# Kernel tuning notes

Measured on AMD Instinct MI355X. Metric: run time of the kernel, lower is better.

The kernel has to match this reference:

```python
import jax, jax.numpy as jnp
import numpy as np
from jax import lax

C = 128; G = 8; K = 3; P = K * K; GC = C // G
N, H, W = 4, 96, 96
EPS = 1e-5

def conv_bn_silu(x, w, gamma, beta, rmean, rvar, stride, pad):
    # Conv2d(bias=False) + BatchNorm2d(eval) + SiLU, NCHW
    y = lax.conv_general_dilated(x, w, (stride, stride), [(pad, pad), (pad, pad)],
                                 dimension_numbers=('NCHW', 'OIHW', 'NCHW'))
    s = gamma / jnp.sqrt(rvar + EPS)
    y = y * s[None, :, None, None] + (beta - rmean * s)[None, :, None, None]
    return y * jax.nn.sigmoid(y)

def dcnv3(x, dw_w, dw_b, ln_g, ln_b, off_w, off_b, m_w, m_b, ip_w, ip_b, op_w, op_b):
    # InternImage DCNv3, channels-last input (N,H,W,C), k=3 s=1 pad=1 dil=1 group=G, offset_scale=1
    n, h, w, c = x.shape
    xp = x @ ip_w.T + ip_b  # input_proj
    # offset/mask branch: depthwise 3x3 conv + LayerNorm + GELU on the ORIGINAL input
    dw = lax.conv_general_dilated(x, dw_w, (1, 1), [(1, 1), (1, 1)],
                                  dimension_numbers=('NHWC', 'HWIO', 'NHWC'),
                                  feature_group_count=c) + dw_b
    dw = (dw - dw.mean(-1, keepdims=True)) / jnp.sqrt(dw.var(-1, keepdims=True) + EPS) * ln_g + ln_b
    dw = jax.nn.gelu(dw)
    off = (dw @ off_w.T + off_b).reshape(n, h, w, G, P, 2)  # (..., (dx, dy))
    m = jax.nn.softmax((dw @ m_w.T + m_b).reshape(n, h, w, G, P), -1)
    pad = 1
    hp, wp = h + 2 * pad, w + 2 * pad
    xpad = jnp.pad(xp, ((0, 0), (pad, pad), (pad, pad), (0, 0))).reshape(n, hp, wp, G, GC)
    ky, kx = jnp.meshgrid(jnp.arange(-1, 2, dtype=x.dtype), jnp.arange(-1, 2, dtype=x.dtype), indexing='ij')
    # absolute sampling coords in padded image (grid_sample align_corners=False equivalent)
    py = (jnp.arange(h, dtype=x.dtype) + pad)[None, :, None, None, None] + ky.reshape(-1) + off[..., 1]
    px = (jnp.arange(w, dtype=x.dtype) + pad)[None, None, :, None, None] + kx.reshape(-1) + off[..., 0]
    yf = jnp.floor(py); xf = jnp.floor(px)
    wy = py - yf; wx = px - xf
    y0 = yf.astype(jnp.int32); x0 = xf.astype(jnp.int32)
    n_idx = jnp.arange(n)[:, None, None, None, None]
    g_idx = jnp.arange(G)[None, None, None, :, None]

    def gat(yi, xi):
        valid = ((yi >= 0) & (yi < hp) & (xi >= 0) & (xi < wp)).astype(x.dtype)
        v = xpad[n_idx, jnp.clip(yi, 0, hp - 1), jnp.clip(xi, 0, wp - 1), g_idx]  # (n,h,w,G,P,GC)
        return v * valid[..., None]

    v = (gat(y0, x0) * ((1 - wy) * (1 - wx))[..., None]
         + gat(y0, x0 + 1) * ((1 - wy) * wx)[..., None]
         + gat(y0 + 1, x0) * (wy * (1 - wx))[..., None]
         + gat(y0 + 1, x0 + 1) * (wy * wx)[..., None])
    out = jnp.einsum('nhwgpc,nhwgp->nhwgc', v, m).reshape(n, h, w, c)
    return out @ op_w.T + op_b  # output_proj

def _forward(x0, x1, x2, conv_w, conv_g, conv_b, conv_rm, conv_rv,
             conv1_w, conv1_g, conv1_b, conv1_rm, conv1_rv,
             conv2_w, conv2_g, conv2_b, conv2_rm, conv2_rv,
             dw_w, dw_b, ln_g, ln_b, off_w, off_b, m_w, m_b, ip_w, ip_b, op_w, op_b):
    n, _, h, w = x0.shape
    # x1: 256 ch > 128 -> self.conv (1x1); smaller spatial -> bilinear upsample to HW
    y1 = conv_bn_silu(x1, conv_w, conv_g, conv_b, conv_rm, conv_rv, 1, 0)
    feat_up1 = jax.image.resize(y1, (n, C, h, w), method='bilinear')
    # x2: 64 ch < 128 -> self.conv1 (1x1); larger spatial -> self.conv2 (3x3 s2) to HW
    y2 = conv_bn_silu(x2, conv1_w, conv1_g, conv1_b, conv1_rm, conv1_rv, 1, 0)
    feat_up2 = conv_bn_silu(y2, conv2_w, conv2_g, conv2_b, conv2_rm, conv2_rv, 2, 1)
    d1 = dcnv3(feat_up1.transpose(0, 2, 3, 1), dw_w, dw_b, ln_g, ln_b, off_w, off_b, m_w, m_b, ip_w, ip_b, op_w, op_b)
    d2 = dcnv3(feat_up2.transpose(0, 2, 3, 1), dw_w, dw_b, ln_g, ln_b, off_w, off_b, m_w, m_b, ip_w, ip_b, op_w, op_b)
    a1 = jax.nn.relu(d1).transpose(0, 3, 1, 2)
    a2 = jax.nn.relu(d2).transpose(0, 3, 1, 2)
    return jnp.concatenate([a1, x0, a2], axis=1)  # (N, 3C, H, W)

def setup_inputs():
    ks = jax.random.split(jax.random.key(0), 24)
    f = jnp.float32
    return {
        'x0': jax.random.normal(ks[0], (N, C, H, W), f),
        'x1': jax.random.normal(ks[1], (N, 2 * C, H // 2, W // 2), f),
        'x2': jax.random.normal(ks[2], (N, C // 2, 2 * H, 2 * W), f),
        'conv_w': jax.random.normal(ks[3], (C, 2 * C, 1, 1), f) * 0.05,
        'conv_g': jnp.ones((C,), f), 'conv_b': jnp.zeros((C,), f),
        'conv_rm': jax.random.normal(ks[4], (C,), f) * 0.1,
        'conv_rv': jax.random.uniform(ks[5], (C,), f) + 0.5,
        'conv1_w': jax.random.normal(ks[6], (C, C // 2, 1, 1), f) * 0.08,
        'conv1_g': jnp.ones((C,), f), 'conv1_b': jnp.zeros((C,), f),
        'conv1_rm': jax.random.normal(ks[7], (C,), f) * 0.1,
        'conv1_rv': jax.random.uniform(ks[8], (C,), f) + 0.5,
        'conv2_w': jax.random.normal(ks[9], (C, C, 3, 3), f) * 0.03,
        'conv2_g': jnp.ones((C,), f), 'conv2_b': jnp.zeros((C,), f),
        'conv2_rm': jax.random.normal(ks[10], (C,), f) * 0.1,
        'conv2_rv': jax.random.uniform(ks[11], (C,), f) + 0.5,
        'dw_w': jax.random.normal(ks[12], (3, 3, 1, C), f) * 0.1,
        'dw_b': jnp.zeros((C,), f),
        'ln_g': jnp.ones((C,), f), 'ln_b': jnp.zeros((C,), f),
        'off_w': jax.random.normal(ks[13], (G * P * 2, C), f) * 0.01,
        'off_b': jnp.zeros((G * P * 2,), f),
        'm_w': jax.random.normal(ks[14], (G * P, C), f) * 0.05,
        'm_b': jnp.zeros((G * P,), f),
        'ip_w': jax.random.normal(ks[15], (C, C), f) * 0.05,
        'ip_b': jnp.zeros((C,), f),
        'op_w': jax.random.normal(ks[16], (C, C), f) * 0.05,
        'op_b': jnp.zeros((C,), f),
    }

def reference(x0, x1, x2, conv_w, conv_g, conv_b, conv_rm, conv_rv,
              conv1_w, conv1_g, conv1_b, conv1_rm, conv1_rv,
              conv2_w, conv2_g, conv2_b, conv2_rm, conv2_rv,
              dw_w, dw_b, ln_g, ln_b, off_w, off_b, m_w, m_b, ip_w, ip_b, op_w, op_b):
    return _forward(x0, x1, x2, conv_w, conv_g, conv_b, conv_rm, conv_rv,
                    conv1_w, conv1_g, conv1_b, conv1_rm, conv1_rv,
                    conv2_w, conv2_g, conv2_b, conv2_rm, conv2_rv,
                    dw_w, dw_b, ln_g, ln_b, off_w, off_b, m_w, m_b, ip_w, ip_b, op_w, op_b)
```

## Files before the change

kernel.cpp:

```cpp
#include <hip/hip_runtime.h>
#include <cstdint>
#include <cstddef>

#define EPSV 1e-5f
#define NPIX 9216
#define LDA 136
#define LDK 72

typedef __bf16 bf16;
typedef __attribute__((ext_vector_type(8))) __bf16 bf16x8;
typedef __attribute__((ext_vector_type(4))) __bf16 bf16x4;
typedef __attribute__((ext_vector_type(4))) float  f32x4;

__device__ __forceinline__ float silu_f(float v) { return v / (1.f + __expf(-v)); }

__global__ __launch_bounds__(256) void prep_kernel(
    const float* __restrict__ conv_w, const float* __restrict__ conv_g,
    const float* __restrict__ conv_b, const float* __restrict__ conv_rm, const float* __restrict__ conv_rv,
    const float* __restrict__ conv1_w, const float* __restrict__ conv1_g,
    const float* __restrict__ conv1_b, const float* __restrict__ conv1_rm, const float* __restrict__ conv1_rv,
    const float* __restrict__ conv2_w, const float* __restrict__ conv2_g,
    const float* __restrict__ conv2_bb, const float* __restrict__ conv2_rm, const float* __restrict__ conv2_rv,
    const float* __restrict__ ip_w, const float* __restrict__ op_w,
    const float* __restrict__ off_w, const float* __restrict__ m_w,
    const float* __restrict__ off_b, const float* __restrict__ m_b,
    float* __restrict__ WTSf, bf16* __restrict__ WTSb)
{
  int idx = blockIdx.x * 256 + threadIdx.x;
  if (idx < 608) {
    if (idx < 128) {
      int co = idx;
      float s = conv_g[co] * rsqrtf(conv_rv[co] + EPSV);
      WTSf[idx] = conv_b[co] - conv_rm[co] * s;
    } else if (idx < 256) {
      int co = idx - 128;
      float s = conv1_g[co] * rsqrtf(conv1_rv[co] + EPSV);
      WTSf[idx] = conv1_b[co] - conv1_rm[co] * s;
    } else if (idx < 384) {
      int co = idx - 256;
      float s = conv2_g[co] * rsqrtf(conv2_rv[co] + EPSV);
      WTSf[idx] = conv2_bb[co] - conv2_rm[co] * s;
    } else {
      int col = idx - 384;
      WTSf[idx] = (col < 144) ? off_b[col] : (col < 216 ? m_b[col - 144] : 0.f);
    }
  } else {
    int j = idx - 608;
    if (j < 32768) {
      int co = j >> 8, ci = j & 255;
      float s = conv_g[co] * rsqrtf(conv_rv[co] + EPSV);
      WTSb[j] = (bf16)(conv_w[co * 256 + ci] * s);
    } else if (j < 40960) {
      int r = j - 32768; int co = r >> 6, ci = r & 63;
      float s = conv1_g[co] * rsqrtf(conv1_rv[co] + EPSV);
      WTSb[j] = (bf16)(conv1_w[co * 64 + ci] * s);
    } else if (j < 188416) {
      int r = j - 40960; int kp = r >> 14; int rr = r & 16383;
      int co = rr >> 7, ci = rr & 127;
      float s = conv2_g[co] * rsqrtf(conv2_rv[co] + EPSV);
      WTSb[j] = (bf16)(conv2_w[(co * 128 + ci) * 9 + kp] * s);
    } else if (j < 204800) {
      int r = j - 188416; int co = r >> 7, ci = r & 127;
      WTSb[j] = (bf16)ip_w[co * 128 + ci];
    } else if (j < 233472) {
      int r = j - 204800; int co = r >> 7, ci = r & 127;
      float v = (co < 144) ? off_w[co * 128 + ci] : (co < 216 ? m_w[(co - 144) * 128 + ci] : 0.f);
      WTSb[j] = (bf16)v;
    } else if (j < 249856) {
      int r = j - 233472; int co = r >> 7, ci = r & 127;
      WTSb[j] = (bf16)op_w[co * 128 + ci];
    }
  }
}

__global__ __launch_bounds__(256) void c1x1_mfma_kernel(
    const float* __restrict__ x, const bf16* __restrict__ W,
    const float* __restrict__ bias, int K, int HW, bf16* __restrict__ outb)
{
  __shared__ bf16 As[64 * LDK];
  __shared__ bf16 Bs[128 * LDK];
  int m0 = blockIdx.x << 6;
  int t = threadIdx.x;
  int n = m0 / HW; int hw0 = m0 - n * HW;
  const float* xn = x + (size_t)n * K * HW;
  int wv = t >> 6, lane = t & 63;
  int lrow = lane & 15, q = lane >> 4;
  int n0 = wv * 32;
  f32x4 acc[4][2];
#pragma unroll
  for (int i = 0; i < 4; ++i)
#pragma unroll
    for (int j = 0; j < 2; ++j)
#pragma unroll
      for (int e = 0; e < 4; ++e) acc[i][j][e] = 0.f;

  for (int k0 = 0; k0 < K; k0 += 64) {
    if (k0) __syncthreads();
    for (int i = t; i < 1024; i += 256) {
      int px = i & 63; int ci4 = (i >> 6) << 2;
      bf16x4 p;
#pragma unroll
      for (int j = 0; j < 4; ++j)
        p[j] = (bf16)xn[(size_t)(k0 + ci4 + j) * HW + hw0 + px];
      *(bf16x4*)&As[px * LDK + ci4] = p;
    }
    for (int i = t; i < 1024; i += 256) {
      int co = i >> 3; int k8 = (i & 7) << 3;
      *(bf16x8*)&Bs[co * LDK + k8] = *(const bf16x8*)&W[(size_t)co * K + k0 + k8];
    }
    __syncthreads();
#pragma unroll
    for (int ks = 0; ks < 2; ++ks) {
      int ko = ks * 32 + q * 8;
      bf16x8 bfr0 = *(const bf16x8*)&Bs[(n0 + lrow) * LDK + ko];
      bf16x8 bfr1 = *(const bf16x8*)&Bs[(n0 + 16 + lrow) * LDK + ko];
#pragma unroll
      for (int mi = 0; mi < 4; ++mi) {
        bf16x8 afr = *(const bf16x8*)&As[(mi * 16 + lrow) * LDK + ko];
        acc[mi][0] = __builtin_amdgcn_mfma_f32_16x16x32_bf16(afr, bfr0, acc[mi][0], 0, 0, 0);
        acc[mi][1] = __builtin_amdgcn_mfma_f32_16x16x32_bf16(afr, bfr1, acc[mi][1], 0, 0, 0);
      }
    }
  }
#pragma unroll
  for (int mi = 0; mi < 4; ++mi) {
#pragma unroll
    for (int nj = 0; nj < 2; ++nj) {
      int co = n0 + nj * 16 + lrow;
      float bb = bias[co];
#pragma unroll
      for (int r = 0; r < 4; ++r) {
        int m = m0 + mi * 16 + q * 4 + r;
        outb[(size_t)m * 128 + co] = (bf16)silu_f(acc[mi][nj][r] + bb);
      }
    }
  }
}

__global__ __launch_bounds__(256) void upsample_kernel(
    const bf16* __restrict__ y1b, bf16* __restrict__ feat1b)
{
  int idx = blockIdx.x * 256 + threadIdx.x;
  int c4 = (idx & 31) << 2;
  int pw = idx >> 5;
  int ow = pw % 96; int t1 = pw / 96;
  int oh = t1 % 96; int n = t1 / 96;
  float sh = oh * 0.5f - 0.25f, sw = ow * 0.5f - 0.25f;
  float hf = floorf(sh), wf = floorf(sw);
  float fy = sh - hf, fx = sw - wf;
  int h0 = (int)hf, w0 = (int)wf;
  int h0c = max(h0, 0), h1c = min(h0 + 1, 47);
  int w0c = max(w0, 0), w1c = min(w0 + 1, 47);
  const bf16* yn = y1b + (size_t)n * 2304 * 128 + c4;
  bf16x4 v00 = *(const bf16x4*)&yn[(h0c * 48 + w0c) * 128];
  bf16x4 v01 = *(const bf16x4*)&yn[(h0c * 48 + w1c) * 128];
  bf16x4 v10 = *(const bf16x4*)&yn[(h1c * 48 + w0c) * 128];
  bf16x4 v11 = *(const bf16x4*)&yn[(h1c * 48 + w1c) * 128];
  bf16x4 o;
#pragma unroll
  for (int e = 0; e < 4; ++e) {
    float v = (1.f - fy) * ((1.f - fx) * (float)v00[e] + fx * (float)v01[e])
            + fy * ((1.f - fx) * (float)v10[e] + fx * (float)v11[e]);
    o[e] = (bf16)v;
  }
  *(bf16x4*)&feat1b[((size_t)n * NPIX + oh * 96 + ow) * 128 + c4] = o;
}

__global__ __launch_bounds__(256) void conv2_mfma_kernel(
    const bf16* __restrict__ y2b, const bf16* __restrict__ W2b,
    const float* __restrict__ b2, bf16* __restrict__ feat2b)
{
  __shared__ bf16 As[64 * LDA];
  __shared__ bf16 Bs[128 * LDA];
  int m0 = blockIdx.x << 6;
  int t = threadIdx.x;
  int wv = t >> 6, lane = t & 63;
  int lrow = lane & 15, q = lane >> 4;
  int n0 = wv * 32;
  f32x4 acc[4][2];
#pragma unroll
  for (int i = 0; i < 4; ++i)
#pragma unroll
    for (int j = 0; j < 2; ++j)
#pragma unroll
      for (int e = 0; e < 4; ++e) acc[i][j][e] = 0.f;
  bf16x8 zv;
#pragma unroll
  for (int e = 0; e < 8; ++e) zv[e] = (bf16)0.f;

  for (int kp = 0; kp < 9; ++kp) {
    int kh = kp / 3, kw = kp - kh * 3;
    __syncthreads();
    for (int i = t; i < 1024; i += 256) {
      int row = i >> 4; int c8 = (i & 15) << 3;
      int m = m0 + row;
      int nimg = m / NPIX; int hw = m - nimg * NPIX;
      int oh = hw / 96, ow = hw - oh * 96;
      int ih = 2 * oh - 1 + kh, iw = 2 * ow - 1 + kw;
      bf16x8 v = zv;
      if ((unsigned)ih < 192u && (unsigned)iw < 192u)
        v = *(const bf16x8*)&y2b[(((size_t)nimg * 192 + ih) * 192 + iw) * 128 + c8];
      *(bf16x8*)&As[row * LDA + c8] = v;
    }
    const bf16* Wk = W2b + kp * 16384;
    for (int i = t; i < 2048; i += 256) {
      int nn = i >> 4; int k8 = (i & 15) << 3;
      *(bf16x8*)&Bs[nn * LDA + k8] = *(const bf16x8*)&Wk[nn * 128 + k8];
    }
    __syncthreads();
#pragma unroll
    for (int ks = 0; ks < 4; ++ks) {
      bf16x8 bfr0 = *(const bf16x8*)&Bs[(n0 + lrow) * LDA + ks * 32 + q * 8];
      bf16x8 bfr1 = *(const bf16x8*)&Bs[(n0 + 16 + lrow) * LDA + ks * 32 + q * 8];
#pragma unroll
      for (int mi = 0; mi < 4; ++mi) {
        bf16x8 afr = *(const bf16x8*)&As[(mi * 16 + lrow) * LDA + ks * 32 + q * 8];
        acc[mi][0] = __builtin_amdgcn_mfma_f32_16x16x32_bf16(afr, bfr0, acc[mi][0], 0, 0, 0);
        acc[mi][1] = __builtin_amdgcn_mfma_f32_16x16x32_bf16(afr, bfr1, acc[mi][1], 0, 0, 0);
      }
    }
  }
#pragma unroll
  for (int mi = 0; mi < 4; ++mi) {
#pragma unroll
    for (int nj = 0; nj < 2; ++nj) {
      int co = n0 + nj * 16 + lrow;
      float bb = b2[co];
#pragma unroll
      for (int r = 0; r < 4; ++r) {
        int m = m0 + mi * 16 + q * 4 + r;
        feat2b[(size_t)m * 128 + co] = (bf16)silu_f(acc[mi][nj][r] + bb);
      }
    }
  }
}

__global__ __launch_bounds__(256) void mm_bf16_kernel(
    const bf16* __restrict__ A, const bf16* __restrict__ W,
    const float* __restrict__ bias, int Nc, int ostride, int act,
    int store_mode, void* __restrict__ outp)
{
  __shared__ bf16 As[64 * LDA];
  __shared__ bf16 Bs[128 * LDA];
  int m0 = blockIdx.x << 6;
  int nb = blockIdx.y << 7;
  int cols_here = Nc - nb; if (cols_here > 128) cols_here = 128;
  int t = threadIdx.x;
  for (int i = t; i < 1024; i += 256) {
    int row = i >> 4; int c8 = (i & 15) << 3;
    *(bf16x8*)&As[row * LDA + c8] = *(const bf16x8*)&A[(size_t)(m0 + row) * 128 + c8];
  }
  bf16x8 zv;
#pragma unroll
  for (int e = 0; e < 8; ++e) zv[e] = (bf16)0.f;
  for (int i = t; i < 2048; i += 256) {
    int n = i >> 4; int k8 = (i & 15) << 3;
    bf16x8 v = (n < cols_here) ? *(const bf16x8*)&W[(size_t)(nb + n) * 128 + k8] : zv;
    *(bf16x8*)&Bs[n * LDA + k8] = v;
  }
  __syncthreads();

  int wv = t >> 6, lane = t & 63;
  int lrow = lane & 15, q = lane >> 4;
  int n0 = wv * 32;
  f32x4 acc[4][2];
#pragma unroll
  for (int i = 0; i < 4; ++i)
#pragma unroll
    for (int j = 0; j < 2; ++j)
#pragma unroll
      for (int e = 0; e < 4; ++e) acc[i][j][e] = 0.f;

#pragma unroll
  for (int ks = 0; ks < 4; ++ks) {
    bf16x8 bfr0 = *(const bf16x8*)&Bs[(n0 + lrow) * LDA + ks * 32 + q * 8];
    bf16x8 bfr1 = *(const bf16x8*)&Bs[(n0 + 16 + lrow) * LDA + ks * 32 + q * 8];
#pragma unroll
    for (int mi = 0; mi < 4; ++mi) {
      bf16x8 afr = *(const bf16x8*)&As[(mi * 16 + lrow) * LDA + ks * 32 + q * 8];
      acc[mi][0] = __builtin_amdgcn_mfma_f32_16x16x32_bf16(afr, bfr0, acc[mi][0], 0, 0, 0);
      acc[mi][1] = __builtin_amdgcn_mfma_f32_16x16x32_bf16(afr, bfr1, acc[mi][1], 0, 0, 0);
    }
  }

  float* outf = (float*)outp;
  bf16*  outb = (bf16*)outp;
#pragma unroll
  for (int mi = 0; mi < 4; ++mi) {
#pragma unroll
    for (int nj = 0; nj < 2; ++nj) {
      int col = nb + n0 + nj * 16 + lrow;
      if (col >= Nc) continue;
      float bb = bias[col];
#pragma unroll
      for (int r = 0; r < 4; ++r) {
        int m = m0 + mi * 16 + q * 4 + r;
        float v = acc[mi][nj][r] + bb;
        if (act == 1) v = fmaxf(v, 0.f);
        if (store_mode == 0) {
          outf[(size_t)m * ostride + col] = v;
        } else if (store_mode == 2) {
          outb[(size_t)m * 128 + col] = (bf16)v;
        } else {
          int nn = m / NPIX; int hw = m - nn * NPIX;
          int img = nn & 3; int choff = (nn >= 4) ? 256 : 0;
          outf[((size_t)(img * 384 + choff + col)) * NPIX + hw] = v;
        }
      }
    }
  }
}

__global__ __launch_bounds__(256) void dwln_kernel(
    const bf16* __restrict__ featb, const float* __restrict__ dw_w,
    const float* __restrict__ dw_b, const float* __restrict__ ln_g,
    const float* __restrict__ ln_b, bf16* __restrict__ dwgb)
{
  int t = threadIdx.x;
  int pxl = t >> 4;
  int c8 = (t & 15) << 3;
  int pixel = blockIdx.x * 16 + pxl;
  int n = pixel / NPIX; int hw = pixel - n * NPIX;
  int h = hw / 96; int w = hw - h * 96;
  const bf16* fn = featb + (size_t)n * NPIX * 128 + c8;
  float acc[8];
#pragma unroll
  for (int e = 0; e < 8; ++e) acc[e] = dw_b[c8 + e];
#pragma unroll
  for (int kh = 0; kh < 3; ++kh) {
    int hh = h + kh - 1;
    if ((unsigned)hh >= 96u) continue;
#pragma unroll
    for (int kw = 0; kw < 3; ++kw) {
      int ww = w + kw - 1;
      if ((unsigned)ww >= 96u) continue;
      bf16x8 v = *(const bf16x8*)&fn[(hh * 96 + ww) * 128];
      const float* wt = &dw_w[(kh * 3 + kw) * 128 + c8];
#pragma unroll
      for (int e = 0; e < 8; ++e) acc[e] += (float)v[e] * wt[e];
    }
  }
  float s = 0.f, qs = 0.f;
#pragma unroll
  for (int e = 0; e < 8; ++e) { s += acc[e]; qs += acc[e] * acc[e]; }
#pragma unroll
  for (int off = 8; off > 0; off >>= 1) {
    s  += __shfl_xor(s, off);
    qs += __shfl_xor(qs, off);
  }
  float mean = s * (1.f / 128.f);
  float var = qs * (1.f / 128.f) - mean * mean;
  float rstd = rsqrtf(var + EPSV);
  bf16x8 o;
#pragma unroll
  for (int e = 0; e < 8; ++e) {
    float xn = (acc[e] - mean) * rstd * ln_g[c8 + e] + ln_b[c8 + e];
    float z = 0.7978845608028654f * (xn + 0.044715f * xn * xn * xn);
    float th;
    if (z > 15.f) th = 1.f;
    else if (z < -15.f) th = -1.f;
    else { float e2 = __expf(2.f * z); th = (e2 - 1.f) / (e2 + 1.f); }
    o[e] = (bf16)(0.5f * xn * (1.f + th));
  }
  *(bf16x8*)&dwgb[(size_t)pixel * 128 + c8] = o;
}

__global__ __launch_bounds__(256) void sample_kernel(
    const bf16* __restrict__ xpb, const float* __restrict__ offm,
    bf16* __restrict__ vaggb)
{
  __shared__ float S[16 * 224];
  int t = threadIdx.x;
  int bid = blockIdx.x;
  for (int i = t; i < 3584; i += 256) S[i] = offm[(size_t)bid * 3584 + i];
  __syncthreads();
  int pxl = t >> 4;
  int tid16 = t & 15;
  int g = tid16 >> 1;
  int c8 = (tid16 & 1) << 3;
  int pixel = bid * 16 + pxl;
  int n = pixel / NPIX; int hw = pixel - n * NPIX;
  int h = hw / 96; int w = hw - h * 96;
  const float* Sp = S + pxl * 224;
  float lg[9]; float mx = -1e30f;
#pragma unroll
  for (int p = 0; p < 9; ++p) { lg[p] = Sp[144 + g * 9 + p]; mx = fmaxf(mx, lg[p]); }
  float se = 0.f;
#pragma unroll
  for (int p = 0; p < 9; ++p) { lg[p] = __expf(lg[p] - mx); se += lg[p]; }
  float inv = 1.f / se;
  const bf16* xpn = xpb + (size_t)n * NPIX * 128 + g * 16 + c8;
  float acc[8];
#pragma unroll
  for (int e = 0; e < 8; ++e) acc[e] = 0.f;
#pragma unroll
  for (int p = 0; p < 9; ++p) {
    float dx = Sp[g * 18 + p * 2], dy = Sp[g * 18 + p * 2 + 1];
    float pyu = (float)(h + p / 3 - 1) + dy;
    float pxu = (float)(w + p % 3 - 1) + dx;
    float yf = floorf(pyu), xf = floorf(pxu);
    float wy = pyu - yf, wx = pxu - xf;
    int y0 = (int)yf, x0 = (int)xf;
    float ay0 = ((unsigned)y0 < 96u) ? (1.f - wy) : 0.f;
    float ay1 = ((unsigned)(y0 + 1) < 96u) ? wy : 0.f;
    float ax0 = ((unsigned)x0 < 96u) ? (1.f - wx) : 0.f;
    float ax1 = ((unsigned)(x0 + 1) < 96u) ? wx : 0.f;
    int y0c = min(max(y0, 0), 95), y1c = min(max(y0 + 1, 0), 95);
    int x0c = min(max(x0, 0), 95), x1c = min(max(x0 + 1, 0), 95);
    float w00 = ay0 * ax0, w01 = ay0 * ax1, w10 = ay1 * ax0, w11 = ay1 * ax1;
    bf16x8 v00 = *(const bf16x8*)&xpn[(y0c * 96 + x0c) * 128];
    bf16x8 v01 = *(const bf16x8*)&xpn[(y0c * 96 + x1c) * 128];
    bf16x8 v10 = *(const bf16x8*)&xpn[(y1c * 96 + x0c) * 128];
    bf16x8 v11 = *(const bf16x8*)&xpn[(y1c * 96 + x1c) * 128];
    float mp = lg[p] * inv;
#pragma unroll
    for (int e = 0; e < 8; ++e) {
      float sv = w00 * (float)v00[e] + w01 * (float)v01[e]
               + w10 * (float)v10[e] + w11 * (float)v11[e];
      acc[e] += mp * sv;
    }
  }
  bf16x8 o;
#pragma unroll
  for (int e = 0; e < 8; ++e) o[e] = (bf16)acc[e];
  *(bf16x8*)&vaggb[(size_t)pixel * 128 + g * 16 + c8] = o;
}

__global__ __launch_bounds__(256) void copy_x0_kernel(
    const float4* __restrict__ x0, float4* __restrict__ out)
{
  int idx = blockIdx.x * 256 + threadIdx.x;
  int n = idx / (128 * 2304);
  int r = idx - n * (128 * 2304);
  out[(size_t)(n * 384 + 128) * 2304 + r] = x0[(size_t)n * 128 * 2304 + r];
}

extern "C" void kernel_launch(void* const* d_in, const int* in_sizes, int n_in,
                              void* d_out, int out_size, void* d_ws, size_t ws_size,
                              hipStream_t stream)
{
  (void)in_sizes; (void)n_in; (void)out_size; (void)ws_size;
  const float* x0      = (const float*)d_in[0];
  const float* x1      = (const float*)d_in[1];
  const float* x2      = (const float*)d_in[2];
  const float* conv_w  = (const float*)d_in[3];
  const float* conv_g  = (const float*)d_in[4];
  const float* conv_b  = (const float*)d_in[5];
  const float* conv_rm = (const float*)d_in[6];
  const float* conv_rv = (const float*)d_in[7];
  const float* conv1_w = (const float*)d_in[8];
  const float* conv1_g = (const float*)d_in[9];
  const float* conv1_b = (const float*)d_in[10];
  const float* conv1_rm= (const float*)d_in[11];
  const float* conv1_rv= (const float*)d_in[12];
  const float* conv2_w = (const float*)d_in[13];
  const float* conv2_g = (const float*)d_in[14];
  const float* conv2_b = (const float*)d_in[15];
  const float* conv2_rm= (const float*)d_in[16];
  const float* conv2_rv= (const float*)d_in[17];
  const float* dw_w    = (const float*)d_in[18];
  const float* dw_b    = (const float*)d_in[19];
  const float* ln_g    = (const float*)d_in[20];
  const float* ln_b    = (const float*)d_in[21];
  const float* off_w   = (const float*)d_in[22];
  const float* off_b   = (const float*)d_in[23];
  const float* m_w     = (const float*)d_in[24];
  const float* m_b     = (const float*)d_in[25];
  const float* ip_w    = (const float*)d_in[26];
  const float* ip_b    = (const float*)d_in[27];
  const float* op_w    = (const float*)d_in[28];
  const float* op_b    = (const float*)d_in[29];
  float* out = (float*)d_out;
  char* WS = (char*)d_ws;

  bf16* featb  = (bf16*)WS;
  bf16* feat1b = featb;
  bf16* feat2b = featb + 4718592;
  bf16* y2b    = (bf16*)(WS + 18874368);
  bf16* xpb    = (bf16*)(WS + 18874368);
  bf16* dwgb   = (bf16*)(WS + 37748736);
  bf16* vaggb  = dwgb;
  bf16* y1b    = (bf16*)(WS + 56623104);
  float* offm  = (float*)(WS + 58982400);
  float* WTSf  = (float*)(WS + 125042688);
  bf16*  WTSb  = (bf16*)(WS + 125045120);

  float* b1f  = WTSf;
  float* b1bf = WTSf + 128;
  float* b2f  = WTSf + 256;
  float* bomf = WTSf + 384;
  bf16* W1b  = WTSb;
  bf16* W1bb = WTSb + 32768;
  bf16* W2b  = WTSb + 40960;
  bf16* Wipb = WTSb + 188416;
  bf16* Womb = WTSb + 204800;
  bf16* Wopb = WTSb + 233472;

  prep_kernel<<<979, 256, 0, stream>>>(
      conv_w, conv_g, conv_b, conv_rm, conv_rv,
      conv1_w, conv1_g, conv1_b, conv1_rm, conv1_rv,
      conv2_w, conv2_g, conv2_b, conv2_rm, conv2_rv,
      ip_w, op_w, off_w, m_w, off_b, m_b, WTSf, WTSb);

  c1x1_mfma_kernel<<<144, 256, 0, stream>>>(x1, W1b, b1f, 256, 2304, y1b);
  upsample_kernel<<<4608, 256, 0, stream>>>(y1b, feat1b);

  c1x1_mfma_kernel<<<2304, 256, 0, stream>>>(x2, W1bb, b1bf, 64, 36864, y2b);
  conv2_mfma_kernel<<<576, 256, 0, stream>>>(y2b, W2b, b2f, feat2b);

  mm_bf16_kernel<<<dim3(1152, 1), 256, 0, stream>>>(featb, Wipb, ip_b, 128, 128, 0, 2, xpb);
  dwln_kernel<<<4608, 256, 0, stream>>>(featb, dw_w, dw_b, ln_g, ln_b, dwgb);
  mm_bf16_kernel<<<dim3(1152, 2), 256, 0, stream>>>(dwgb, Womb, bomf, 224, 224, 0, 0, offm);
  sample_kernel<<<4608, 256, 0, stream>>>(xpb, offm, vaggb);
  mm_bf16_kernel<<<dim3(1152, 1), 256, 0, stream>>>(vaggb, Wopb, op_b, 128, 0, 1, 1, out);

  copy_x0_kernel<<<4608, 256, 0, stream>>>((const float4*)x0, (float4*)out);
}
```

Baseline: 431.7 us.

## Fuse offset/mask GEMM, deformable sampling and output projection into one kernel

Replaces three launches (offset/mask GEMM, sampling kernel, output-projection GEMM) with one kernel that works on 64-pixel tiles. The offset/mask logits are kept in fp16 shared memory and the sampled values stay in shared memory as the A operand of the output GEMM. This removes the global round trips of the fp32 offm buffer and the bf16 vagg buffer. In exchange it uses much more LDS per block, which lowers occupancy, and it serialises the GEMM and gather phases inside each block; storing the offsets in fp16 also reduces their precision.

```diff
diff --git a/kernel.cpp b/kernel.cpp
--- a/kernel.cpp
+++ b/kernel.cpp
@@ -6,6 +6,7 @@
 #define NPIX 9216
 #define LDA 136
 #define LDK 72
+#define SPX 66
 
 typedef __bf16 bf16;
 typedef __attribute__((ext_vector_type(8))) __bf16 bf16x8;
@@ -365,65 +366,157 @@
   *(bf16x8*)&dwgb[(size_t)pixel * 128 + c8] = o;
 }
 
-__global__ __launch_bounds__(256) void sample_kernel(
-    const bf16* __restrict__ xpb, const float* __restrict__ offm,
-    bf16* __restrict__ vaggb)
-{
-  __shared__ float S[16 * 224];
+__global__ __launch_bounds__(256) void omsop_kernel(
+    const bf16* __restrict__ dwgb, const bf16* __restrict__ xpb,
+    const bf16* __restrict__ Womb, const float* __restrict__ bomf,
+    const bf16* __restrict__ Wopb, const float* __restrict__ opb,
+    float* __restrict__ out)
+{
+  __shared__ bf16 As[64 * LDA];
+  __shared__ bf16 Bs[64 * LDA];
+  __shared__ _Float16 S[224 * SPX];
+  int m0 = blockIdx.x << 6;
   int t = threadIdx.x;
-  int bid = blockIdx.x;
-  for (int i = t; i < 3584; i += 256) S[i] = offm[(size_t)bid * 3584 + i];
+  int wv = t >> 6, lane = t & 63;
+  int lrow = lane & 15, q = lane >> 4;
+  bf16x8 zv;
+#pragma unroll
+  for (int e = 0; e < 8; ++e) zv[e] = (bf16)0.f;
+
+  for (int i = t; i < 1024; i += 256) {
+    int row = i >> 4, c8 = (i & 15) << 3;
+    *(bf16x8*)&As[row * LDA + c8] = *(const bf16x8*)&dwgb[(size_t)(m0 + row) * 128 + c8];
+  }
   __syncthreads();
-  int pxl = t >> 4;
-  int tid16 = t & 15;
-  int g = tid16 >> 1;
-  int c8 = (tid16 & 1) << 3;
-  int pixel = bid * 16 + pxl;
-  int n = pixel / NPIX; int hw = pixel - n * NPIX;
-  int h = hw / 96; int w = hw - h * 96;
-  const float* Sp = S + pxl * 224;
-  float lg[9]; float mx = -1e30f;
-#pragma unroll
-  for (int p = 0; p < 9; ++p) { lg[p] = Sp[144 + g * 9 + p]; mx = fmaxf(mx, lg[p]); }
-  float se = 0.f;
-#pragma unroll
-  for (int p = 0; p < 9; ++p) { lg[p] = __expf(lg[p] - mx); se += lg[p]; }
-  float inv = 1.f / se;
-  const bf16* xpn = xpb + (size_t)n * NPIX * 128 + g * 16 + c8;
-  float acc[8];
-#pragma unroll
-  for (int e = 0; e < 8; ++e) acc[e] = 0.f;
-#pragma unroll
-  for (int p = 0; p < 9; ++p) {
-    float dx = Sp[g * 18 + p * 2], dy = Sp[g * 18 + p * 2 + 1];
-    float pyu = (float)(h + p / 3 - 1) + dy;
-    float pxu = (float)(w + p % 3 - 1) + dx;
-    float yf = floorf(pyu), xf = floorf(pxu);
-    float wy = pyu - yf, wx = pxu - xf;
-    int y0 = (int)yf, x0 = (int)xf;
-    float ay0 = ((unsigned)y0 < 96u) ? (1.f - wy) : 0.f;
-    float ay1 = ((unsigned)(y0 + 1) < 96u) ? wy : 0.f;
-    float ax0 = ((unsigned)x0 < 96u) ? (1.f - wx) : 0.f;
-    float ax1 = ((unsigned)(x0 + 1) < 96u) ? wx : 0.f;
-    int y0c = min(max(y0, 0), 95), y1c = min(max(y0 + 1, 0), 95);
-    int x0c = min(max(x0, 0), 95), x1c = min(max(x0 + 1, 0), 95);
-    float w00 = ay0 * ax0, w01 = ay0 * ax1, w10 = ay1 * ax0, w11 = ay1 * ax1;
-    bf16x8 v00 = *(const bf16x8*)&xpn[(y0c * 96 + x0c) * 128];
-    bf16x8 v01 = *(const bf16x8*)&xpn[(y0c * 96 + x1c) * 128];
-    bf16x8 v10 = *(const bf16x8*)&xpn[(y1c * 96 + x0c) * 128];
-    bf16x8 v11 = *(const bf16x8*)&xpn[(y1c * 96 + x1c) * 128];
-    float mp = lg[p] * inv;
-#pragma unroll
-    for (int e = 0; e < 8; ++e) {
-      float sv = w00 * (float)v00[e] + w01 * (float)v01[e]
-               + w10 * (float)v10[e] + w11 * (float)v11[e];
-      acc[e] += mp * sv;
-    }
-  }
-  bf16x8 o;
-#pragma unroll
-  for (int e = 0; e < 8; ++e) o[e] = (bf16)acc[e];
-  *(bf16x8*)&vaggb[(size_t)pixel * 128 + g * 16 + c8] = o;
+
+  for (int c = 0; c < 4; ++c) {
+    for (int i = t; i < 1024; i += 256) {
+      int rr = i >> 4, k8 = (i & 15) << 3;
+      int gr = c * 64 + rr;
+      bf16x8 v = (gr < 224) ? *(const bf16x8*)&Womb[(size_t)gr * 128 + k8] : zv;
+      *(bf16x8*)&Bs[rr * LDA + k8] = v;
+    }
+    __syncthreads();
+    f32x4 acc[4];
+#pragma unroll
+    for (int mi = 0; mi < 4; ++mi)
+#pragma unroll
+      for (int e = 0; e < 4; ++e) acc[mi][e] = 0.f;
+#pragma unroll
+    for (int ks = 0; ks < 4; ++ks) {
+      bf16x8 bfr = *(const bf16x8*)&Bs[(wv * 16 + lrow) * LDA + ks * 32 + q * 8];
+#pragma unroll
+      for (int mi = 0; mi < 4; ++mi) {
+        bf16x8 afr = *(const bf16x8*)&As[(mi * 16 + lrow) * LDA + ks * 32 + q * 8];
+        acc[mi] = __builtin_amdgcn_mfma_f32_16x16x32_bf16(afr, bfr, acc[mi], 0, 0, 0);
+      }
+    }
+    int col = c * 64 + wv * 16 + lrow;
+    if (col < 224) {
+      float bb = bomf[col];
+#pragma unroll
+      for (int mi = 0; mi < 4; ++mi)
+#pragma unroll
+        for (int r = 0; r < 4; ++r)
+          S[col * SPX + mi * 16 + q * 4 + r] = (_Float16)(acc[mi][r] + bb);
+    }
+    __syncthreads();
+  }
+
+  {
+    int gg = (t >> 1) & 7;
+    int c8s = (t & 1) << 3;
+    for (int k = 0; k < 4; ++k) {
+      int px = (t >> 4) + (k << 4);
+      int pixel = m0 + px;
+      int n = pixel / NPIX; int hw = pixel - n * NPIX;
+      int h = hw / 96, w = hw - h * 96;
+      float lg[9]; float mx = -1e30f;
+#pragma unroll
+      for (int p = 0; p < 9; ++p) {
+        lg[p] = (float)S[(144 + gg * 9 + p) * SPX + px];
+        mx = fmaxf(mx, lg[p]);
+      }
+      float se = 0.f;
+#pragma unroll
+      for (int p = 0; p < 9; ++p) { lg[p] = __expf(lg[p] - mx); se += lg[p]; }
+      float inv = 1.f / se;
+      const bf16* xpn = xpb + (size_t)n * NPIX * 128 + gg * 16 + c8s;
+      float acc8[8];
+#pragma unroll
+      for (int e = 0; e < 8; ++e) acc8[e] = 0.f;
+#pragma unroll
+      for (int p = 0; p < 9; ++p) {
+        float dx = (float)S[(gg * 18 + p * 2) * SPX + px];
+        float dy = (float)S[(gg * 18 + p * 2 + 1) * SPX + px];
+        float pyu = (float)(h + p / 3 - 1) + dy;
+        float pxu = (float)(w + p % 3 - 1) + dx;
+        float yf = floorf(pyu), xf = floorf(pxu);
+        float wy = pyu - yf, wx = pxu - xf;
+        int y0 = (int)yf, x0 = (int)xf;
+        float ay0 = ((unsigned)y0 < 96u) ? (1.f - wy) : 0.f;
+        float ay1 = ((unsigned)(y0 + 1) < 96u) ? wy : 0.f;
+        float ax0 = ((unsigned)x0 < 96u) ? (1.f - wx) : 0.f;
+        float ax1 = ((unsigned)(x0 + 1) < 96u) ? wx : 0.f;
+        int y0c = min(max(y0, 0), 95), y1c = min(max(y0 + 1, 0), 95);
+        int x0c = min(max(x0, 0), 95), x1c = min(max(x0 + 1, 0), 95);
+        float w00 = ay0 * ax0, w01 = ay0 * ax1, w10 = ay1 * ax0, w11 = ay1 * ax1;
+        bf16x8 v00 = *(const bf16x8*)&xpn[(y0c * 96 + x0c) * 128];
+        bf16x8 v01 = *(const bf16x8*)&xpn[(y0c * 96 + x1c) * 128];
+        bf16x8 v10 = *(const bf16x8*)&xpn[(y1c * 96 + x0c) * 128];
+        bf16x8 v11 = *(const bf16x8*)&xpn[(y1c * 96 + x1c) * 128];
+        float mp = lg[p] * inv;
+#pragma unroll
+        for (int e = 0; e < 8; ++e) {
+          float sv = w00 * (float)v00[e] + w01 * (float)v01[e]
+                   + w10 * (float)v10[e] + w11 * (float)v11[e];
+          acc8[e] += mp * sv;
+        }
+      }
+      bf16x8 o;
+#pragma unroll
+      for (int e = 0; e < 8; ++e) o[e] = (bf16)acc8[e];
+      *(bf16x8*)&As[px * LDA + gg * 16 + c8s] = o;
+    }
+  }
+  __syncthreads();
+
+  for (int c2 = 0; c2 < 2; ++c2) {
+    for (int i = t; i < 1024; i += 256) {
+      int rr = i >> 4, k8 = (i & 15) << 3;
+      *(bf16x8*)&Bs[rr * LDA + k8] =
+          *(const bf16x8*)&Wopb[(size_t)(c2 * 64 + rr) * 128 + k8];
+    }
+    __syncthreads();
+    f32x4 acc[4];
+#pragma unroll
+    for (int mi = 0; mi < 4; ++mi)
+#pragma unroll
+      for (int e = 0; e < 4; ++e) acc[mi][e] = 0.f;
+#pragma unroll
+    for (int ks = 0; ks < 4; ++ks) {
+      bf16x8 bfr = *(const bf16x8*)&Bs[(wv * 16 + lrow) * LDA + ks * 32 + q * 8];
+#pragma unroll
+      for (int mi = 0; mi < 4; ++mi) {
+        bf16x8 afr = *(const bf16x8*)&As[(mi * 16 + lrow) * LDA + ks * 32 + q * 8];
+        acc[mi] = __builtin_amdgcn_mfma_f32_16x16x32_bf16(afr, bfr, acc[mi], 0, 0, 0);
+      }
+    }
+    int col = c2 * 64 + wv * 16 + lrow;
+    float bb = opb[col];
+#pragma unroll
+    for (int mi = 0; mi < 4; ++mi) {
+#pragma unroll
+      for (int r = 0; r < 4; ++r) {
+        int m = m0 + mi * 16 + q * 4 + r;
+        float v = fmaxf(acc[mi][r] + bb, 0.f);
+        int nn = m / NPIX; int hww = m - nn * NPIX;
+        int img = nn & 3; int choff = (nn >= 4) ? 256 : 0;
+        out[((size_t)(img * 384 + choff + col)) * NPIX + hww] = v;
+      }
+    }
+    __syncthreads();
+  }
 }
 
 __global__ __launch_bounds__(256) void copy_x0_kernel(
@@ -479,9 +572,7 @@
   bf16* y2b    = (bf16*)(WS + 18874368);
   bf16* xpb    = (bf16*)(WS + 18874368);
   bf16* dwgb   = (bf16*)(WS + 37748736);
-  bf16* vaggb  = dwgb;
   bf16* y1b    = (bf16*)(WS + 56623104);
-  float* offm  = (float*)(WS + 58982400);
   float* WTSf  = (float*)(WS + 125042688);
   bf16*  WTSb  = (bf16*)(WS + 125045120);
 
@@ -510,9 +601,7 @@
 
   mm_bf16_kernel<<<dim3(1152, 1), 256, 0, stream>>>(featb, Wipb, ip_b, 128, 128, 0, 2, xpb);
   dwln_kernel<<<4608, 256, 0, stream>>>(featb, dw_w, dw_b, ln_g, ln_b, dwgb);
-  mm_bf16_kernel<<<dim3(1152, 2), 256, 0, stream>>>(dwgb, Womb, bomf, 224, 224, 0, 0, offm);
-  sample_kernel<<<4608, 256, 0, stream>>>(xpb, offm, vaggb);
-  mm_bf16_kernel<<<dim3(1152, 1), 256, 0, stream>>>(vaggb, Wopb, op_b, 128, 0, 1, 1, out);
+  omsop_kernel<<<1152, 256, 0, stream>>>(dwgb, xpb, Womb, bomf, Wopb, op_b, out);
 
   copy_x0_kernel<<<4608, 256, 0, stream>>>((const float4*)x0, (float4*)out);
 }
```

Result: no change. 433.0 us (+0.3%).
